# Kernel optimization log

Hardware: AMD Instinct MI355X
Metric: run time of the kernel (lower is better)

The kernel has to match this reference:

```python
import jax, jax.numpy as jnp
import numpy as np

N_SLICES, H, W = 64, 64, 64
VD, VH, VW = 64, 64, 64
K = 3            # PSF kernel size per axis
RES = 1.5        # res_s / res_r
GAP = 1.0        # through-plane slice spacing in recon voxels
N_ITER = 2       # CG iterations (init kwarg)


def _rotmat(ax, ay, az):
    cx, sx = np.cos(ax), np.sin(ax)
    cy, sy = np.cos(ay), np.sin(ay)
    cz, sz = np.cos(az), np.sin(az)
    Rx = np.array([[1, 0, 0], [0, cx, -sx], [0, sx, cx]])
    Ry = np.array([[cy, 0, sy], [0, 1, 0], [-sy, 0, cy]])
    Rz = np.array([[cz, -sz, 0], [sz, cz, 0], [0, 0, 1]])
    return Rz @ Ry @ Rx


def setup_inputs() -> dict:
    rng = np.random.default_rng(0)
    R = np.stack([_rotmat(*rng.normal(0.0, 0.05, 3)) for _ in range(N_SLICES)])
    t = np.zeros((N_SLICES, 3))
    t[:, :2] = rng.normal(0.0, 1.0, (N_SLICES, 2))
    t[:, 2] = (np.arange(N_SLICES) - (N_SLICES - 1) / 2) * GAP + rng.normal(0.0, 0.3, N_SLICES)
    transforms = jnp.asarray(np.concatenate([R, t[:, :, None]], -1), jnp.float32)  # (S,3,4)
    k1, k2 = jax.random.split(jax.random.key(0))
    slices = jax.random.uniform(k1, (N_SLICES, H, W), jnp.float32)
    volume = jax.random.uniform(k2, (VD, VH, VW), jnp.float32) * 0.1
    g = np.arange(K) - (K - 1) / 2
    gz, gy, gx = np.meshgrid(g, g, g, indexing='ij')
    psf = np.exp(-(gx ** 2 + gy ** 2) / (2 * 0.6 ** 2) - gz ** 2 / (2 * 1.0 ** 2))
    psf = jnp.asarray(psf / psf.sum(), jnp.float32)
    return {"transforms": transforms, "slices": slices, "volume": volume, "psf": psf}


def _positions(transforms):
    # PSF sample positions of every slice pixel, mapped into volume voxel coords (xyz).
    xs = (jnp.arange(W) - (W - 1) / 2) * RES
    ys = (jnp.arange(H) - (H - 1) / 2) * RES
    o = jnp.arange(K) - (K - 1) / 2
    oz, oy, ox = jnp.meshgrid(o, o, o, indexing='ij')
    off = jnp.stack([ox, oy, oz], -1).reshape(-1, 3)              # (K^3, 3)
    base = jnp.stack(jnp.broadcast_arrays(xs[None, :], ys[:, None], jnp.zeros((H, W))), -1)
    pts = base[None] + off[:, None, None, :]                      # (K^3, H, W, 3) slice frame
    R, tr = transforms[:, :, :3], transforms[:, :, 3]
    pos = jnp.einsum('sij,khwj->skhwi', R, pts) + tr[:, None, None, None, :]
    center = jnp.array([(VW - 1) / 2, (VH - 1) / 2, (VD - 1) / 2], jnp.float32)
    return pos + center                                           # (S, K^3, H, W, 3)


def _corner_iter(pos):
    # yields the 8 trilinear corners: (clipped int indices (z,y,x), weight with OOB zeroed)
    x, y, z = pos[..., 0], pos[..., 1], pos[..., 2]
    x0, y0, z0 = jnp.floor(x), jnp.floor(y), jnp.floor(z)
    fx, fy, fz = x - x0, y - y0, z - z0
    for dz in (0, 1):
        for dy in (0, 1):
            for dx in (0, 1):
                xi, yi, zi = x0 + dx, y0 + dy, z0 + dz
                w = (fx if dx else 1 - fx) * (fy if dy else 1 - fy) * (fz if dz else 1 - fz)
                valid = (xi >= 0) & (xi < VW) & (yi >= 0) & (yi < VH) & (zi >= 0) & (zi < VD)
                w = jnp.where(valid, w, 0.0)
                yield (jnp.clip(zi, 0, VD - 1).astype(jnp.int32),
                       jnp.clip(yi, 0, VH - 1).astype(jnp.int32),
                       jnp.clip(xi, 0, VW - 1).astype(jnp.int32)), w


def _A(vol, pos, psf_flat):
    # slice_acquisition: trilinear gather + PSF-weighted sum -> (S,H,W)
    acc = jnp.zeros(pos.shape[:-1], vol.dtype)
    for (zi, yi, xi), w in _corner_iter(pos):
        acc = acc + w * vol[zi, yi, xi]
    return jnp.einsum('k,skhw->shw', psf_flat, acc)


def _At(slc, pos, psf_flat):
    # slice_acquisition_adjoint: PSF-weighted trilinear scatter-add -> (VD,VH,VW)
    vals = psf_flat[None, :, None, None] * slc[:, None]           # (S,K^3,H,W)
    vol = jnp.zeros((VD, VH, VW), slc.dtype)
    for (zi, yi, xi), w in _corner_iter(pos):
        vol = vol.at[zi, yi, xi].add(w * vals)
    return vol


def _cg(Afun, b, x0, n_iter):
    x = x0
    r = b - Afun(x)
    p = r
    rr = jnp.vdot(r, r)
    for i in range(n_iter):
        Ap = Afun(p)
        alpha = rr / jnp.vdot(p, Ap)
        x = x + alpha * p
        if i == n_iter - 1:
            break
        r = r - alpha * Ap
        rr_new = jnp.vdot(r, r)
        p = r + (rr_new / rr) * p
        rr = rr_new
    return x


def reference(transforms, slices, volume, psf):
    pos = _positions(transforms)
    psf_flat = psf.reshape(-1)
    AtA = lambda v: _At(_A(v, pos, psf_flat), pos, psf_flat)
    b = _At(slices, pos, psf_flat)
    x = _cg(AtA, b, volume, N_ITER)
    return jax.nn.relu(x)
```

## Files before the change

kernel.cpp:

```cpp
#include <hip/hip_runtime.h>

#define NS 64
#define HH 64
#define WW 64
#define VD 64
#define VH 64
#define VW 64
#define NVOX (VD*VH*VW)
#define NPIX (NS*HH*WW)
#define RES 1.5f
#define NTAB (NS*27)
#define WIN 6
#define SPLIT 8
#define COL_PAD 67
#define GP_ROW 68
#define GP_SLC (66*GP_ROW)
#define GP_TOT (NS*GP_SLC)

__global__ __launch_bounds__(256) void k_setup(const float* __restrict__ tr,
                                               const float* __restrict__ psf,
                                               float* __restrict__ tab) {
    int i = blockIdx.x * 256 + threadIdx.x;
    if (i >= NTAB) return;
    int s = i / 27, k = i % 27;
    const float* p = tr + s * 12;
    float R00 = p[0], R01 = p[1], R02 = p[2],  t0 = p[3];
    float R10 = p[4], R11 = p[5], R12 = p[6],  t1 = p[7];
    float R20 = p[8], R21 = p[9], R22 = p[10], t2 = p[11];
    float Ux = RES * R00, Uy = RES * R10, Uz = RES * R20;
    float Vx = RES * R01, Vy = RES * R11, Vz = RES * R21;
    float ox = (float)(k % 3 - 1), oy = (float)((k / 3) % 3 - 1), oz = (float)(k / 9 - 1);
    float Cx = t0 + 31.5f + R00 * ox + R01 * oy + R02 * oz - 31.5f * (Ux + Vx);
    float Cy = t1 + 31.5f + R10 * ox + R11 * oy + R12 * oz - 31.5f * (Uy + Vy);
    float Cz = t2 + 31.5f + R20 * ox + R21 * oy + R22 * oz - 31.5f * (Uz + Vz);
    float inv = 1.f / (Ux * Vy - Uy * Vx);
    float* e = tab + i * 16;
    e[0] = Vy * inv;  e[1] = -Uy * inv;  e[2] = -Vx * inv; e[3] = Ux * inv;
    e[4] = Ux; e[5] = Uy; e[6] = Vx; e[7] = Vy;
    e[8] = Uz; e[9] = Vz; e[10] = Cx; e[11] = Cy;
    e[12] = Cz; e[13] = psf[k]; e[14] = 0.f; e[15] = 0.f;
}

__device__ __forceinline__ float trilin_gather_bf(const float* __restrict__ vol,
                                                  float px, float py, float pz) {
    float x0 = floorf(px), y0 = floorf(py), z0 = floorf(pz);
    float fx = px - x0, fy = py - y0, fz = pz - z0;
    int ix = (int)x0, iy = (int)y0, iz = (int)z0;

    float wx0 = ((unsigned)ix       < 64u) ? (1.f - fx) : 0.f;
    float wx1 = ((unsigned)(ix + 1) < 64u) ? fx         : 0.f;
    float wy0 = ((unsigned)iy       < 64u) ? (1.f - fy) : 0.f;
    float wy1 = ((unsigned)(iy + 1) < 64u) ? fy         : 0.f;
    float wz0 = ((unsigned)iz       < 64u) ? (1.f - fz) : 0.f;
    float wz1 = ((unsigned)(iz + 1) < 64u) ? fz         : 0.f;

    int xc0 = min(max(ix, 0), 63),     xc1 = min(max(ix + 1, 0), 63);
    int yc0 = min(max(iy, 0), 63) << 6,  yc1 = min(max(iy + 1, 0), 63) << 6;
    int zc0 = min(max(iz, 0), 63) << 12, zc1 = min(max(iz + 1, 0), 63) << 12;

    float v000 = vol[zc0 + yc0 + xc0], v001 = vol[zc0 + yc0 + xc1];
    float v010 = vol[zc0 + yc1 + xc0], v011 = vol[zc0 + yc1 + xc1];
    float v100 = vol[zc1 + yc0 + xc0], v101 = vol[zc1 + yc0 + xc1];
    float v110 = vol[zc1 + yc1 + xc0], v111 = vol[zc1 + yc1 + xc1];

    float w00 = wx0 * wy0, w01 = wx1 * wy0, w10 = wx0 * wy1, w11 = wx1 * wy1;
    float lo = fmaf(w00, v000, fmaf(w01, v001, fmaf(w10, v010, w11 * v011)));
    float hi = fmaf(w00, v100, fmaf(w01, v101, fmaf(w10, v110, w11 * v111)));
    return fmaf(wz0, lo, wz1 * hi);
}

template<bool SUB>
__global__ __launch_bounds__(256) void k_a(const float* __restrict__ vin,
                                           float* __restrict__ gp,
                                           const float* __restrict__ tr,
                                           const float* __restrict__ psf,
                                           const float* __restrict__ slc) {
    __shared__ float s_psf[27];
    if (threadIdx.x < 27) s_psf[threadIdx.x] = psf[threadIdx.x];
    __syncthreads();
    int gid = blockIdx.x * 256 + threadIdx.x;
    int s = gid >> 12;
    int h = (gid >> 6) & 63, w = gid & 63;
    const float* p = tr + s * 12;
    float R0 = p[0], R1 = p[1], R2 = p[2],  t0 = p[3];
    float R3 = p[4], R4 = p[5], R5 = p[6],  t1 = p[7];
    float R6 = p[8], R7 = p[9], R8 = p[10], t2 = p[11];
    float xs = ((float)w - 31.5f) * RES;
    float ys = ((float)h - 31.5f) * RES;
    float p0x = fmaf(R0, xs, fmaf(R1, ys, t0)) + 31.5f;
    float p0y = fmaf(R3, xs, fmaf(R4, ys, t1)) + 31.5f;
    float p0z = fmaf(R6, xs, fmaf(R7, ys, t2)) + 31.5f;
    float a = 0.f;
#pragma unroll
    for (int k = 0; k < 27; ++k) {
        const float ox = (float)(k % 3 - 1), oy = (float)((k / 3) % 3 - 1), oz = (float)(k / 9 - 1);
        float px = p0x + ox * R0 + oy * R1 + oz * R2;
        float py = p0y + ox * R3 + oy * R4 + oz * R5;
        float pz = p0z + ox * R6 + oy * R7 + oz * R8;
        bool inb = (px > -1.f) & (px < 64.f) & (py > -1.f) & (py < 64.f)
                 & (pz > -1.f) & (pz < 64.f);
        if (inb) a = fmaf(s_psf[k], trilin_gather_bf(vin, px, py, pz), a);
    }
    float outv = SUB ? (slc[gid] - a) : a;
    gp[s * GP_SLC + (h + 1) * GP_ROW + (w + 1)] = outv;
}

__device__ __forceinline__ void block_reduce_atomic(float v, float* dst) {
#pragma unroll
    for (int off = 32; off > 0; off >>= 1) v += __shfl_down(v, off, 64);
    __shared__ float s_red[4];
    int lane = threadIdx.x & 63, wid = threadIdx.x >> 6;
    if (lane == 0) s_red[wid] = v;
    __syncthreads();
    if (threadIdx.x == 0) atomicAdd(dst, s_red[0] + s_red[1] + s_red[2] + s_red[3]);
}

__global__ __launch_bounds__(512, 2) void k_atv(const float* __restrict__ g,
                                                float* __restrict__ part,
                                                const float* __restrict__ tab) {
    __shared__ float cols[64][COL_PAD];
    int tid = threadIdx.x;
    {
        float4* c4 = (float4*)&cols[0][0];
#pragma unroll
        for (int i = 0; i < 3; ++i) {
            int j = tid + i * 512;
            if (j < 1072) c4[j] = make_float4(0.f, 0.f, 0.f, 0.f);
        }
    }
    __syncthreads();

    int Yb    = blockIdx.x >> 3;
    int split = blockIdx.x & 7;
    int lane  = tid & 63;
    int wave  = tid >> 6;
    int s = __builtin_amdgcn_readfirstlane(split * 8 + wave);
    float X = (float)lane, Y = (float)Yb;

    const float* tb = tab + s * 27 * 16;
    int gbase = s * GP_SLC;

    const float* ec = tb + 13 * 16;
    float4 ce0 = *(const float4*)(ec);
    float4 ce2 = *(const float4*)(ec + 8);
    float4 ce3 = *(const float4*)(ec + 12);
    float rxc = X - ce2.z, ryc = Y - ce2.w;
    float wsc = ce0.x * rxc + ce0.z * ryc;
    float hsc = ce0.y * rxc + ce0.w * ryc;
    float pzc = fmaf(wsc, ce2.x, fmaf(hsc, ce2.y, ce3.x));
    float basef = floorf(pzc) - 2.f;
    int   basei = (int)basef;

    float acc[WIN];
#pragma unroll
    for (int j = 0; j < WIN; ++j) acc[j] = 0.f;

#pragma unroll 3
    for (int k = 0; k < 27; ++k) {
        const float* e = tb + k * 16;
        float4 e0 = *(const float4*)(e);
        float4 e1 = *(const float4*)(e + 4);
        float4 e2 = *(const float4*)(e + 8);
        float4 e3 = *(const float4*)(e + 12);
        float rx = X - e2.z, ry = Y - e2.w;
        float ws = e0.x * rx + e0.z * ry;
        float hs = e0.y * rx + e0.w * ry;
        float w0f = __builtin_amdgcn_fmed3f(floorf(ws), -1.f, 63.f);
        float h0f = __builtin_amdgcn_fmed3f(floorf(hs), -1.f, 63.f);
        int wA = (int)w0f, hA = (int)h0f;
        float Ux = e1.x, Uy = e1.y, Vx = e1.z, Vy = e1.w;
        float Uz = e2.x, Vz = e2.y;
        float Czb = e3.x - basef;
        float psfk = e3.y;
        float Cxr = -rx, Cyr = -ry;
        int colbase = gbase + wA + 1;
#pragma unroll
        for (int dh = 0; dh < 2; ++dh) {
            float fh = h0f + (float)dh;
            float tx  = fmaf(fh, Vx, Cxr);
            float ty  = fmaf(fh, Vy, Cyr);
            float tzb = fmaf(fh, Vz, Czb);
            int rowoff = colbase + (hA + 1 + dh) * GP_ROW;
#pragma unroll
            for (int dw = 0; dw < 2; ++dw) {
                float fw = w0f + (float)dw;
                float ddx = fmaf(fw, Ux, tx);
                float ddy = fmaf(fw, Uy, ty);
                float wx = fmaxf(1.f - fabsf(ddx), 0.f);
                float wy = fmaxf(1.f - fabsf(ddy), 0.f);
                float gv = g[rowoff + dw];
                float val = wx * wy * psfk * gv;
                float prel = fmaf(fw, Uz, tzb);
#pragma unroll
                for (int j = 0; j < WIN; ++j) {
                    float t = fmaxf(0.f, 1.f - fabsf(prel - (float)j));
                    acc[j] = fmaf(val, t, acc[j]);
                }
            }
        }
    }

#pragma unroll
    for (int j = 0; j < WIN; ++j) {
        int zj = basei + j;
        int okz = ((unsigned)zj < 64u);
        int zc = min(max(zj, 0), 63);
        atomicAdd(&cols[lane][zc], okz ? acc[j] : 0.f);
    }
    __syncthreads();

    float* pout = part + split * NVOX + (Yb << 6);
#pragma unroll
    for (int i = 0; i < 8; ++i) {
        int j = tid + i * 512;
        int z = j >> 6, x = j & 63;
        pout[(z << 12) + x] = cols[x][z];
    }
}


__device__ __forceinline__ float sum8(const float* __restrict__ part, int i) {
    float a = 0.f;
#pragma unroll
    for (int j = 0; j < SPLIT; ++j) a += part[j * NVOX + i];
    return a;
}

__global__ __launch_bounds__(256) void k_residual8(const float* __restrict__ part,
                                                   float* __restrict__ r,
                                                   float* __restrict__ p,
                                                   float* __restrict__ scal) {
    int i = blockIdx.x * 256 + threadIdx.x;
    float rv = sum8(part, i);
    r[i] = rv;
    p[i] = rv;
    block_reduce_atomic(rv * rv, &scal[0]);
}

__global__ __launch_bounds__(256) void k_dot_reduce8(const float* __restrict__ part,
                                                     const float* __restrict__ p,
                                                     float* __restrict__ Ap,
                                                     float* __restrict__ dst) {
    int i = blockIdx.x * 256 + threadIdx.x;
    float apv = sum8(part, i);
    Ap[i] = apv;
    block_reduce_atomic(p[i] * apv, dst);
}

__global__ __launch_bounds__(256) void k_dot8(const float* __restrict__ part,
                                              const float* __restrict__ p,
                                              float* __restrict__ dst) {
    int i = blockIdx.x * 256 + threadIdx.x;
    block_reduce_atomic(p[i] * sum8(part, i), dst);
}

__global__ __launch_bounds__(256) void k_update_xr(const float* __restrict__ x_in,
                                                   float* __restrict__ x_out,
                                                   float* __restrict__ r,
                                                   const float* __restrict__ p,
                                                   const float* __restrict__ Ap,
                                                   float* __restrict__ scal) {
    int i = blockIdx.x * 256 + threadIdx.x;
    float alpha = scal[0] / scal[1];
    x_out[i] = fmaf(alpha, p[i], x_in[i]);
    float rv = fmaf(-alpha, Ap[i], r[i]);
    r[i] = rv;
    block_reduce_atomic(rv * rv, &scal[2]);
}

__global__ __launch_bounds__(256) void k_update_p(float* __restrict__ p,
                                                  const float* __restrict__ r,
                                                  const float* __restrict__ scal) {
    int i = blockIdx.x * 256 + threadIdx.x;
    float beta = scal[2] / scal[0];
    p[i] = fmaf(beta, p[i], r[i]);
}

__global__ __launch_bounds__(256) void k_final(const float* __restrict__ x,
                                               const float* __restrict__ p,
                                               const float* __restrict__ scal,
                                               float* __restrict__ out) {
    int i = blockIdx.x * 256 + threadIdx.x;
    float alpha = scal[2] / scal[3];
    float v = fmaf(alpha, p[i], x[i]);
    out[i] = v > 0.f ? v : 0.f;
}

extern "C" void kernel_launch(void* const* d_in, const int* in_sizes, int n_in,
                              void* d_out, int out_size, void* d_ws, size_t ws_size,
                              hipStream_t stream) {
    const float* transforms = (const float*)d_in[0];
    const float* slices     = (const float*)d_in[1];
    const float* volume     = (const float*)d_in[2];
    const float* psf        = (const float*)d_in[3];
    float* out = (float*)d_out;

    float* tab    = (float*)d_ws;
    float* gbuf   = tab    + NTAB * 16;
    float* scal   = gbuf   + GP_TOT;
    float* part   = scal   + 8;
    float* vol_x  = part   + SPLIT * NVOX;
    float* vol_r  = vol_x  + NVOX;
    float* vol_p  = vol_r  + NVOX;
    float* Ap     = vol_p  + NVOX;

    const int ablk = 64 * SPLIT;
    const int fblk = NPIX / 256;
    const int vblk = NVOX / 256;

    hipMemsetAsync(gbuf, 0, (GP_TOT + 8) * sizeof(float), stream);

    k_setup<<<(NTAB + 255) / 256, 256, 0, stream>>>(transforms, psf, tab);

    k_a<true><<<fblk, 256, 0, stream>>>(volume, gbuf, transforms, psf, slices);
    k_atv<<<ablk, 512, 0, stream>>>(gbuf, part, tab);
    k_residual8<<<vblk, 256, 0, stream>>>(part, vol_r, vol_p, scal);

    k_a<false><<<fblk, 256, 0, stream>>>(vol_p, gbuf, transforms, psf, nullptr);
    k_atv<<<ablk, 512, 0, stream>>>(gbuf, part, tab);
    k_dot_reduce8<<<vblk, 256, 0, stream>>>(part, vol_p, Ap, &scal[1]);
    k_update_xr<<<vblk, 256, 0, stream>>>(volume, vol_x, vol_r, vol_p, Ap, scal);
    k_update_p<<<vblk, 256, 0, stream>>>(vol_p, vol_r, scal);

    k_a<false><<<fblk, 256, 0, stream>>>(vol_p, gbuf, transforms, psf, nullptr);
    k_atv<<<ablk, 512, 0, stream>>>(gbuf, part, tab);
    k_dot8<<<vblk, 256, 0, stream>>>(part, vol_p, &scal[3]);
    k_final<<<vblk, 256, 0, stream>>>(vol_x, vol_p, scal, out);
}
```

Before: 273.1 us.

## Fuse whole CG pipeline into one cooperative persistent kernel with grid syncs

```diff
diff --git a/kernel.cpp b/kernel.cpp
--- a/kernel.cpp
+++ b/kernel.cpp
@@ -1,4 +1,7 @@
 #include <hip/hip_runtime.h>
+#include <hip/hip_cooperative_groups.h>
+
+namespace cg = cooperative_groups;
 
 #define NS 64
 #define HH 64
@@ -16,12 +19,12 @@
 #define GP_ROW 68
 #define GP_SLC (66*GP_ROW)
 #define GP_TOT (NS*GP_SLC)
-
-__global__ __launch_bounds__(256) void k_setup(const float* __restrict__ tr,
-                                               const float* __restrict__ psf,
-                                               float* __restrict__ tab) {
-    int i = blockIdx.x * 256 + threadIdx.x;
-    if (i >= NTAB) return;
+#define NBLK 512
+#define NTHR 512
+
+__device__ __forceinline__ void setup_entry(int i, const float* __restrict__ tr,
+                                            const float* __restrict__ psf,
+                                            float* __restrict__ tab) {
     int s = i / 27, k = i % 27;
     const float* p = tr + s * 12;
     float R00 = p[0], R01 = p[1], R02 = p[2],  t0 = p[3];
@@ -70,15 +73,12 @@
 }
 
 template<bool SUB>
-__global__ __launch_bounds__(256) void k_a(const float* __restrict__ vin,
-                                           float* __restrict__ gp,
-                                           const float* __restrict__ tr,
-                                           const float* __restrict__ psf,
-                                           const float* __restrict__ slc) {
-    __shared__ float s_psf[27];
-    if (threadIdx.x < 27) s_psf[threadIdx.x] = psf[threadIdx.x];
-    __syncthreads();
-    int gid = blockIdx.x * 256 + threadIdx.x;
+__device__ __forceinline__ void phase_a(const float* __restrict__ vin,
+                                        float* __restrict__ gp,
+                                        const float* __restrict__ tr,
+                                        const float* __restrict__ psf,
+                                        const float* __restrict__ slc,
+                                        int gid) {
     int s = gid >> 12;
     int h = (gid >> 6) & 63, w = gid & 63;
     const float* p = tr + s * 12;
@@ -99,27 +99,17 @@
         float pz = p0z + ox * R6 + oy * R7 + oz * R8;
         bool inb = (px > -1.f) & (px < 64.f) & (py > -1.f) & (py < 64.f)
                  & (pz > -1.f) & (pz < 64.f);
-        if (inb) a = fmaf(s_psf[k], trilin_gather_bf(vin, px, py, pz), a);
+        if (inb) a = fmaf(psf[k], trilin_gather_bf(vin, px, py, pz), a);
     }
     float outv = SUB ? (slc[gid] - a) : a;
     gp[s * GP_SLC + (h + 1) * GP_ROW + (w + 1)] = outv;
 }
 
-__device__ __forceinline__ void block_reduce_atomic(float v, float* dst) {
-#pragma unroll
-    for (int off = 32; off > 0; off >>= 1) v += __shfl_down(v, off, 64);
-    __shared__ float s_red[4];
-    int lane = threadIdx.x & 63, wid = threadIdx.x >> 6;
-    if (lane == 0) s_red[wid] = v;
-    __syncthreads();
-    if (threadIdx.x == 0) atomicAdd(dst, s_red[0] + s_red[1] + s_red[2] + s_red[3]);
-}
-
-__global__ __launch_bounds__(512, 2) void k_atv(const float* __restrict__ g,
-                                                float* __restrict__ part,
-                                                const float* __restrict__ tab) {
-    __shared__ float cols[64][COL_PAD];
-    int tid = threadIdx.x;
+__device__ __forceinline__ void phase_atv(const float* __restrict__ g,
+                                          float* __restrict__ part,
+                                          const float* __restrict__ tab,
+                                          int bid, int tid,
+                                          float cols[64][COL_PAD]) {
     {
         float4* c4 = (float4*)&cols[0][0];
 #pragma unroll
@@ -130,8 +120,8 @@
     }
     __syncthreads();
 
-    int Yb    = blockIdx.x >> 3;
-    int split = blockIdx.x & 7;
+    int Yb    = bid >> 3;
+    int split = bid & 7;
     int lane  = tid & 63;
     int wave  = tid >> 6;
     int s = __builtin_amdgcn_readfirstlane(split * 8 + wave);
@@ -218,12 +208,128 @@
     }
 }
 
-
 __device__ __forceinline__ float sum8(const float* __restrict__ part, int i) {
     float a = 0.f;
 #pragma unroll
     for (int j = 0; j < SPLIT; ++j) a += part[j * NVOX + i];
     return a;
+}
+
+__device__ __forceinline__ void bred512(float v, float* dst, float* s_red, int tid) {
+#pragma unroll
+    for (int off = 32; off > 0; off >>= 1) v += __shfl_down(v, off, 64);
+    int lane = tid & 63, wid = tid >> 6;
+    if (lane == 0) s_red[wid] = v;
+    __syncthreads();
+    if (tid == 0) {
+        float t = 0.f;
+#pragma unroll
+        for (int j = 0; j < 8; ++j) t += s_red[j];
+        atomicAdd(dst, t);
+    }
+    __syncthreads();
+}
+
+__global__ __launch_bounds__(512, 4) void mega(const float* __restrict__ tr,
+                                               const float* __restrict__ slices,
+                                               const float* __restrict__ volume,
+                                               const float* __restrict__ psf,
+                                               float* __restrict__ out,
+                                               float* tab, float* gbuf, float* scal,
+                                               float* part, float* vol_x,
+                                               float* vol_r, float* vol_p, float* Ap) {
+    cg::grid_group grid = cg::this_grid();
+    __shared__ float cols[64][COL_PAD];
+    __shared__ float s_red[8];
+    int tid = threadIdx.x;
+    int bid = blockIdx.x;
+    int gidx = bid * NTHR + tid;
+
+    if (gidx < NTAB) setup_entry(gidx, tr, psf, tab);
+    for (int i = gidx; i < GP_TOT + 8; i += NBLK * NTHR) gbuf[i] = 0.f;
+    grid.sync();
+
+    phase_a<true>(volume, gbuf, tr, psf, slices, gidx);
+    grid.sync();
+    phase_atv(gbuf, part, tab, bid, tid, cols);
+    grid.sync();
+    {
+        float rv = sum8(part, gidx);
+        vol_r[gidx] = rv;
+        vol_p[gidx] = rv;
+        bred512(rv * rv, &scal[0], s_red, tid);
+    }
+    grid.sync();
+
+    phase_a<false>(vol_p, gbuf, tr, psf, nullptr, gidx);
+    grid.sync();
+    phase_atv(gbuf, part, tab, bid, tid, cols);
+    grid.sync();
+    {
+        float apv = sum8(part, gidx);
+        Ap[gidx] = apv;
+        bred512(vol_p[gidx] * apv, &scal[1], s_red, tid);
+    }
+    grid.sync();
+    {
+        float alpha = scal[0] / scal[1];
+        vol_x[gidx] = fmaf(alpha, vol_p[gidx], volume[gidx]);
+        float rv = fmaf(-alpha, Ap[gidx], vol_r[gidx]);
+        vol_r[gidx] = rv;
+        bred512(rv * rv, &scal[2], s_red, tid);
+    }
+    grid.sync();
+    {
+        float beta = scal[2] / scal[0];
+        vol_p[gidx] = fmaf(beta, vol_p[gidx], vol_r[gidx]);
+    }
+    grid.sync();
+
+    phase_a<false>(vol_p, gbuf, tr, psf, nullptr, gidx);
+    grid.sync();
+    phase_atv(gbuf, part, tab, bid, tid, cols);
+    grid.sync();
+    bred512(vol_p[gidx] * sum8(part, gidx), &scal[3], s_red, tid);
+    grid.sync();
+    {
+        float alpha = scal[2] / scal[3];
+        float v = fmaf(alpha, vol_p[gidx], vol_x[gidx]);
+        out[gidx] = v > 0.f ? v : 0.f;
+    }
+}
+
+
+__global__ __launch_bounds__(256) void k_setup(const float* __restrict__ tr,
+                                               const float* __restrict__ psf,
+                                               float* __restrict__ tab) {
+    int i = blockIdx.x * 256 + threadIdx.x;
+    if (i < NTAB) setup_entry(i, tr, psf, tab);
+}
+
+template<bool SUB>
+__global__ __launch_bounds__(256) void k_a(const float* __restrict__ vin,
+                                           float* __restrict__ gp,
+                                           const float* __restrict__ tr,
+                                           const float* __restrict__ psf,
+                                           const float* __restrict__ slc) {
+    phase_a<SUB>(vin, gp, tr, psf, slc, blockIdx.x * 256 + threadIdx.x);
+}
+
+__global__ __launch_bounds__(512, 2) void k_atv(const float* __restrict__ g,
+                                                float* __restrict__ part,
+                                                const float* __restrict__ tab) {
+    __shared__ float cols[64][COL_PAD];
+    phase_atv(g, part, tab, blockIdx.x, threadIdx.x, cols);
+}
+
+__device__ __forceinline__ void bred256(float v, float* dst) {
+#pragma unroll
+    for (int off = 32; off > 0; off >>= 1) v += __shfl_down(v, off, 64);
+    __shared__ float s_red[4];
+    int lane = threadIdx.x & 63, wid = threadIdx.x >> 6;
+    if (lane == 0) s_red[wid] = v;
+    __syncthreads();
+    if (threadIdx.x == 0) atomicAdd(dst, s_red[0] + s_red[1] + s_red[2] + s_red[3]);
 }
 
 __global__ __launch_bounds__(256) void k_residual8(const float* __restrict__ part,
@@ -232,9 +338,8 @@
                                                    float* __restrict__ scal) {
     int i = blockIdx.x * 256 + threadIdx.x;
     float rv = sum8(part, i);
-    r[i] = rv;
-    p[i] = rv;
-    block_reduce_atomic(rv * rv, &scal[0]);
+    r[i] = rv; p[i] = rv;
+    bred256(rv * rv, &scal[0]);
 }
 
 __global__ __launch_bounds__(256) void k_dot_reduce8(const float* __restrict__ part,
@@ -244,14 +349,14 @@
     int i = blockIdx.x * 256 + threadIdx.x;
     float apv = sum8(part, i);
     Ap[i] = apv;
-    block_reduce_atomic(p[i] * apv, dst);
+    bred256(p[i] * apv, dst);
 }
 
 __global__ __launch_bounds__(256) void k_dot8(const float* __restrict__ part,
                                               const float* __restrict__ p,
                                               float* __restrict__ dst) {
     int i = blockIdx.x * 256 + threadIdx.x;
-    block_reduce_atomic(p[i] * sum8(part, i), dst);
+    bred256(p[i] * sum8(part, i), dst);
 }
 
 __global__ __launch_bounds__(256) void k_update_xr(const float* __restrict__ x_in,
@@ -265,7 +370,7 @@
     x_out[i] = fmaf(alpha, p[i], x_in[i]);
     float rv = fmaf(-alpha, Ap[i], r[i]);
     r[i] = rv;
-    block_reduce_atomic(rv * rv, &scal[2]);
+    bred256(rv * rv, &scal[2]);
 }
 
 __global__ __launch_bounds__(256) void k_update_p(float* __restrict__ p,
@@ -304,12 +409,19 @@
     float* vol_p  = vol_r  + NVOX;
     float* Ap     = vol_p  + NVOX;
 
+    void* args[] = {(void*)&transforms, (void*)&slices, (void*)&volume, (void*)&psf,
+                    (void*)&out, (void*)&tab, (void*)&gbuf, (void*)&scal, (void*)&part,
+                    (void*)&vol_x, (void*)&vol_r, (void*)&vol_p, (void*)&Ap};
+
+    hipError_t err = hipLaunchCooperativeKernel((void*)mega, dim3(NBLK), dim3(NTHR),
+                                                args, 0, stream);
+    if (err == hipSuccess) return;
+
     const int ablk = 64 * SPLIT;
     const int fblk = NPIX / 256;
     const int vblk = NVOX / 256;
 
     hipMemsetAsync(gbuf, 0, (GP_TOT + 8) * sizeof(float), stream);
-
     k_setup<<<(NTAB + 255) / 256, 256, 0, stream>>>(transforms, psf, tab);
 
     k_a<true><<<fblk, 256, 0, stream>>>(volume, gbuf, transforms, psf, slices);
```

Result: slower. 860.7 us (+215.2%).

## Reformulate 2-step CG in Krylov basis and stage slice band in LDS

Applied to the files above, without the earlier changes.

```diff
diff --git a/kernel.cpp b/kernel.cpp
--- a/kernel.cpp
+++ b/kernel.cpp
@@ -16,6 +16,7 @@
 #define GP_ROW 68
 #define GP_SLC (66*GP_ROW)
 #define GP_TOT (NS*GP_SLC)
+#define BAND 16
 
 __global__ __launch_bounds__(256) void k_setup(const float* __restrict__ tr,
                                                const float* __restrict__ psf,
@@ -105,7 +106,7 @@
     gp[s * GP_SLC + (h + 1) * GP_ROW + (w + 1)] = outv;
 }
 
-__device__ __forceinline__ void block_reduce_atomic(float v, float* dst) {
+__device__ __forceinline__ void bred256(float v, float* dst) {
 #pragma unroll
     for (int off = 32; off > 0; off >>= 1) v += __shfl_down(v, off, 64);
     __shared__ float s_red[4];
@@ -115,10 +116,27 @@
     if (threadIdx.x == 0) atomicAdd(dst, s_red[0] + s_red[1] + s_red[2] + s_red[3]);
 }
 
+__device__ __forceinline__ void bred2(float a, float b, float* da, float* db) {
+#pragma unroll
+    for (int off = 32; off > 0; off >>= 1) {
+        a += __shfl_down(a, off, 64);
+        b += __shfl_down(b, off, 64);
+    }
+    __shared__ float s_red[8];
+    int lane = threadIdx.x & 63, wid = threadIdx.x >> 6;
+    if (lane == 0) { s_red[wid] = a; s_red[4 + wid] = b; }
+    __syncthreads();
+    if (threadIdx.x == 0) {
+        atomicAdd(da, (s_red[0] + s_red[1]) + (s_red[2] + s_red[3]));
+        atomicAdd(db, (s_red[4] + s_red[5]) + (s_red[6] + s_red[7]));
+    }
+}
+
 __global__ __launch_bounds__(512, 2) void k_atv(const float* __restrict__ g,
                                                 float* __restrict__ part,
                                                 const float* __restrict__ tab) {
     __shared__ float cols[64][COL_PAD];
+    __shared__ float sgb[8][BAND * GP_ROW];
     int tid = threadIdx.x;
     {
         float4* c4 = (float4*)&cols[0][0];
@@ -128,7 +146,6 @@
             if (j < 1072) c4[j] = make_float4(0.f, 0.f, 0.f, 0.f);
         }
     }
-    __syncthreads();
 
     int Yb    = blockIdx.x >> 3;
     int split = blockIdx.x & 7;
@@ -138,7 +155,35 @@
     float X = (float)lane, Y = (float)Yb;
 
     const float* tb = tab + s * 27 * 16;
-    int gbase = s * GP_SLC;
+
+    float hlo = 1e9f, hhi = -1e9f;
+    if (lane < 27) {
+        const float* e = tb + lane * 16;
+        float c = e[1], d = e[3], Cx = e[10], Cy = e[11];
+        float ryd = d * (Y - Cy);
+        float hs0 = c * (0.f  - Cx) + ryd;
+        float hs1 = c * (63.f - Cx) + ryd;
+        hlo = fminf(hs0, hs1);
+        hhi = fmaxf(hs0, hs1);
+    }
+#pragma unroll
+    for (int off = 32; off > 0; off >>= 1) {
+        hlo = fminf(hlo, __shfl_xor(hlo, off, 64));
+        hhi = fmaxf(hhi, __shfl_xor(hhi, off, 64));
+    }
+    int rlo = (int)__builtin_amdgcn_fmed3f(floorf(hlo), -1.f, 63.f) + 1;
+    int hbase = min(rlo, 66 - BAND);
+
+    {
+        const float4* gs4 = (const float4*)(g + s * GP_SLC + hbase * GP_ROW);
+        float4* sd4 = (float4*)&sgb[wave][0];
+#pragma unroll
+        for (int i = 0; i < 5; ++i) {
+            int j = lane + i * 64;
+            if (j < 272) sd4[j] = gs4[j];
+        }
+    }
+    __syncthreads();
 
     const float* ec = tb + 13 * 16;
     float4 ce0 = *(const float4*)(ec);
@@ -173,14 +218,15 @@
         float Czb = e3.x - basef;
         float psfk = e3.y;
         float Cxr = -rx, Cyr = -ry;
-        int colbase = gbase + wA + 1;
+        int hrel = hA + 1 - hbase;
+        int colb = wA + 1;
 #pragma unroll
         for (int dh = 0; dh < 2; ++dh) {
             float fh = h0f + (float)dh;
             float tx  = fmaf(fh, Vx, Cxr);
             float ty  = fmaf(fh, Vy, Cyr);
             float tzb = fmaf(fh, Vz, Czb);
-            int rowoff = colbase + (hA + 1 + dh) * GP_ROW;
+            int rowoff = (hrel + dh) * GP_ROW + colb;
 #pragma unroll
             for (int dw = 0; dw < 2; ++dw) {
                 float fw = w0f + (float)dw;
@@ -188,7 +234,7 @@
                 float ddy = fmaf(fw, Uy, ty);
                 float wx = fmaxf(1.f - fabsf(ddx), 0.f);
                 float wy = fmaxf(1.f - fabsf(ddy), 0.f);
-                float gv = g[rowoff + dw];
+                float gv = sgb[wave][rowoff + dw];
                 float val = wx * wy * psfk * gv;
                 float prel = fmaf(fw, Uz, tzb);
 #pragma unroll
@@ -226,63 +272,51 @@
     return a;
 }
 
-__global__ __launch_bounds__(256) void k_residual8(const float* __restrict__ part,
-                                                   float* __restrict__ r,
-                                                   float* __restrict__ p,
-                                                   float* __restrict__ scal) {
+__global__ __launch_bounds__(256) void k_r0(const float* __restrict__ part,
+                                            float* __restrict__ r0,
+                                            float* __restrict__ scal) {
     int i = blockIdx.x * 256 + threadIdx.x;
     float rv = sum8(part, i);
-    r[i] = rv;
-    p[i] = rv;
-    block_reduce_atomic(rv * rv, &scal[0]);
-}
-
-__global__ __launch_bounds__(256) void k_dot_reduce8(const float* __restrict__ part,
-                                                     const float* __restrict__ p,
-                                                     float* __restrict__ Ap,
-                                                     float* __restrict__ dst) {
+    r0[i] = rv;
+    bred256(rv * rv, &scal[0]);
+}
+
+__global__ __launch_bounds__(256) void k_k1(const float* __restrict__ part,
+                                            const float* __restrict__ r0,
+                                            float* __restrict__ K1,
+                                            float* __restrict__ scal) {
     int i = blockIdx.x * 256 + threadIdx.x;
     float apv = sum8(part, i);
-    Ap[i] = apv;
-    block_reduce_atomic(p[i] * apv, dst);
-}
-
-__global__ __launch_bounds__(256) void k_dot8(const float* __restrict__ part,
-                                              const float* __restrict__ p,
-                                              float* __restrict__ dst) {
-    int i = blockIdx.x * 256 + threadIdx.x;
-    block_reduce_atomic(p[i] * sum8(part, i), dst);
-}
-
-__global__ __launch_bounds__(256) void k_update_xr(const float* __restrict__ x_in,
-                                                   float* __restrict__ x_out,
-                                                   float* __restrict__ r,
-                                                   const float* __restrict__ p,
-                                                   const float* __restrict__ Ap,
-                                                   float* __restrict__ scal) {
-    int i = blockIdx.x * 256 + threadIdx.x;
-    float alpha = scal[0] / scal[1];
-    x_out[i] = fmaf(alpha, p[i], x_in[i]);
-    float rv = fmaf(-alpha, Ap[i], r[i]);
-    r[i] = rv;
-    block_reduce_atomic(rv * rv, &scal[2]);
-}
-
-__global__ __launch_bounds__(256) void k_update_p(float* __restrict__ p,
-                                                  const float* __restrict__ r,
-                                                  const float* __restrict__ scal) {
-    int i = blockIdx.x * 256 + threadIdx.x;
-    float beta = scal[2] / scal[0];
-    p[i] = fmaf(beta, p[i], r[i]);
-}
-
-__global__ __launch_bounds__(256) void k_final(const float* __restrict__ x,
-                                               const float* __restrict__ p,
-                                               const float* __restrict__ scal,
-                                               float* __restrict__ out) {
-    int i = blockIdx.x * 256 + threadIdx.x;
-    float alpha = scal[2] / scal[3];
-    float v = fmaf(alpha, p[i], x[i]);
+    K1[i] = apv;
+    bred2(r0[i] * apv, apv * apv, &scal[1], &scal[2]);
+}
+
+__global__ __launch_bounds__(256) void k_dots2(const float* __restrict__ part,
+                                               const float* __restrict__ r0,
+                                               const float* __restrict__ K1,
+                                               float* __restrict__ scal) {
+    int i = blockIdx.x * 256 + threadIdx.x;
+    float apv = sum8(part, i);
+    bred2(r0[i] * apv, K1[i] * apv, &scal[3], &scal[4]);
+}
+
+__global__ __launch_bounds__(256) void k_out(const float* __restrict__ x0,
+                                             const float* __restrict__ r0,
+                                             const float* __restrict__ K1,
+                                             const float* __restrict__ scal,
+                                             float* __restrict__ out) {
+    int i = blockIdx.x * 256 + threadIdx.x;
+    float rr0  = scal[0], rK1 = scal[1], K1K1 = scal[2];
+    float rK2  = scal[3], K1K2 = scal[4];
+    float a0   = rr0 / rK1;
+    float rr1  = rr0 - 2.f * a0 * rK1 + a0 * a0 * K1K1;
+    float beta = rr1 / rr0;
+    float ob   = 1.f + beta;
+    float pAp1 = ob * ob * rK1 - ob * a0 * rK2 - a0 * ob * K1K1 + a0 * a0 * K1K2;
+    float a1   = rr1 / pAp1;
+    float c1   = a0 + a1 * ob;
+    float c2   = -a1 * a0;
+    float v = fmaf(c2, K1[i], fmaf(c1, r0[i], x0[i]));
     out[i] = v > 0.f ? v : 0.f;
 }
 
@@ -299,31 +333,27 @@
     float* gbuf   = tab    + NTAB * 16;
     float* scal   = gbuf   + GP_TOT;
     float* part   = scal   + 8;
-    float* vol_x  = part   + SPLIT * NVOX;
-    float* vol_r  = vol_x  + NVOX;
-    float* vol_p  = vol_r  + NVOX;
-    float* Ap     = vol_p  + NVOX;
+    float* r0     = part   + SPLIT * NVOX;
+    float* K1     = r0     + NVOX;
 
     const int ablk = 64 * SPLIT;
     const int fblk = NPIX / 256;
     const int vblk = NVOX / 256;
 
     hipMemsetAsync(gbuf, 0, (GP_TOT + 8) * sizeof(float), stream);
-
     k_setup<<<(NTAB + 255) / 256, 256, 0, stream>>>(transforms, psf, tab);
 
     k_a<true><<<fblk, 256, 0, stream>>>(volume, gbuf, transforms, psf, slices);
     k_atv<<<ablk, 512, 0, stream>>>(gbuf, part, tab);
-    k_residual8<<<vblk, 256, 0, stream>>>(part, vol_r, vol_p, scal);
-
-    k_a<false><<<fblk, 256, 0, stream>>>(vol_p, gbuf, transforms, psf, nullptr);
+    k_r0<<<vblk, 256, 0, stream>>>(part, r0, scal);
+
+    k_a<false><<<fblk, 256, 0, stream>>>(r0, gbuf, transforms, psf, nullptr);
     k_atv<<<ablk, 512, 0, stream>>>(gbuf, part, tab);
-    k_dot_reduce8<<<vblk, 256, 0, stream>>>(part, vol_p, Ap, &scal[1]);
-    k_update_xr<<<vblk, 256, 0, stream>>>(volume, vol_x, vol_r, vol_p, Ap, scal);
-    k_update_p<<<vblk, 256, 0, stream>>>(vol_p, vol_r, scal);
-
-    k_a<false><<<fblk, 256, 0, stream>>>(vol_p, gbuf, transforms, psf, nullptr);
+    k_k1<<<vblk, 256, 0, stream>>>(part, r0, K1, scal);
+
+    k_a<false><<<fblk, 256, 0, stream>>>(K1, gbuf, transforms, psf, nullptr);
     k_atv<<<ablk, 512, 0, stream>>>(gbuf, part, tab);
-    k_dot8<<<vblk, 256, 0, stream>>>(part, vol_p, &scal[3]);
-    k_final<<<vblk, 256, 0, stream>>>(vol_x, vol_p, scal, out);
-}
+    k_dots2<<<vblk, 256, 0, stream>>>(part, r0, K1, scal);
+
+    k_out<<<vblk, 256, 0, stream>>>(volume, r0, K1, scal, out);
+}
```

New measurement: 293.5 us (median of 4 runs). 7.5% more time.
